# Kernel tuning notes

Measured on AMD Instinct MI355X. Metric: run time of the kernel, lower is better.

## Reference

```python
import math
import jax, jax.numpy as jnp
import numpy as np

QDEPTH = 8
WIDTH = 32
HEIGHT = 32
PIXELS = WIDTH * HEIGHT          # 1024
WIRES = int(math.ceil(math.log2(PIXELS)))  # 10, and PIXELS == 2**WIRES exactly
BATCH = 2048


def setup_inputs() -> dict:
    key = jax.random.key(0)
    k1, k2 = jax.random.split(key)
    x = jax.random.normal(k1, (BATCH, 1, WIDTH, HEIGHT), dtype=jnp.float32)
    # torch.randn(weight_shape) * 0.4
    weights = jax.random.normal(k2, (QDEPTH, WIRES, 3), dtype=jnp.float32) * 0.4
    return {"x": x, "weights": weights, "reps": 1}


def _apply_1q(s, U, wire):
    # s: (batch, 2, 2, ..., 2); apply 2x2 unitary U on qubit `wire` (axis wire+1)
    ax = wire + 1
    s = jnp.moveaxis(s, ax, -1)
    s = s @ U.T                      # new[..., i] = sum_j U[i, j] * old[..., j]
    return jnp.moveaxis(s, -1, ax)


def _apply_cnot(s, ctrl, tgt):
    # flip target bit on the control==1 half of the state
    c_ax = ctrl + 1
    t_ax = tgt + 1
    s0 = jnp.take(s, 0, axis=c_ax)
    s1 = jnp.take(s, 1, axis=c_ax)
    t = t_ax - 1 if t_ax > c_ax else t_ax
    s1 = jnp.flip(s1, axis=t)
    return jnp.stack([s0, s1], axis=c_ax)


def _rot_matrix(phi, theta, omega):
    # qml.Rot = RZ(phi) -> RY(theta) -> RZ(omega)
    c = jnp.cos(theta * 0.5)
    sn = jnp.sin(theta * 0.5)
    ep = jnp.exp(-0.5j * (phi + omega))   # e^{-i(phi+omega)/2}
    em = jnp.exp(-0.5j * (phi - omega))   # e^{-i(phi-omega)/2}
    return jnp.stack([
        jnp.stack([ep * c, -jnp.conj(em) * sn]),
        jnp.stack([em * sn, jnp.conj(ep) * c]),
    ]).astype(jnp.complex64)


def _circuit(psi, weights, reps):
    # psi: (batch, 2**WIRES) complex64 normalized state
    b = psi.shape[0]
    s = psi.reshape((b,) + (2,) * WIRES)
    w = jnp.tanh(weights)                 # qw_map.tanh
    # StronglyEntanglingLayers default ranges: r_l = l % (wires-1) + 1
    ranges = [(l % (WIRES - 1)) + 1 for l in range(QDEPTH)]
    for _ in range(reps):
        for l in range(QDEPTH):
            for q in range(WIRES):
                U = _rot_matrix(w[l, q, 0], w[l, q, 1], w[l, q, 2])
                s = _apply_1q(s, U, q)
            r = ranges[l]
            for q in range(WIRES):
                s = _apply_cnot(s, q, (q + r) % WIRES)
    return s.reshape(b, 2 ** WIRES)


def reference(x, weights, reps):
    b = x.shape[0]
    v = x.reshape(b, PIXELS)                       # b 1 w h -> b (w h)
    old_norm = jnp.linalg.norm(v, axis=-1, keepdims=True)
    psi = (v / old_norm).astype(jnp.complex64)     # real amplitudes, zero imag
    out = _circuit(psi, weights, reps)
    out = out * old_norm.astype(jnp.complex64)
    return out.reshape(b, 1, WIDTH, HEIGHT)
```

## Files before the change

kernel.cpp:

```cpp
#include <hip/hip_runtime.h>
#include <math.h>


#define WIRES   10
#define NSTATE  1024
#define QDEPTH  8
#define NBATCH  2048
#define NGATES  (QDEPTH * WIRES)

#define WS_WORDS 1280

__device__ __forceinline__ int perm_g(int j, int r) {
#pragma unroll
    for (int q = WIRES - 1; q >= 0; --q) {
        const int cb = 9 - q;
        const int tb = 9 - ((q + r) % WIRES);
        j ^= ((j >> cb) & 1) << tb;
    }
    return j;
}

__global__ __launch_bounds__(1024) void qprep(
    const float* __restrict__ weights, float* __restrict__ ws)
{
    const int tid = threadIdx.x;
    if (tid < NGATES) {
        const float phi   = tanhf(weights[tid * 3 + 0]);
        const float theta = tanhf(weights[tid * 3 + 1]);
        const float omega = tanhf(weights[tid * 3 + 2]);
        const float c  = cosf(theta * 0.5f);
        const float sn = sinf(theta * 0.5f);
        const float a  = 0.5f * (phi + omega);
        const float bb = 0.5f * (phi - omega);
        const float ca = cosf(a),  sa = sinf(a);
        const float cb = cosf(bb), sb = sinf(bb);
        ws[tid * 8 + 0] =  ca * c;  ws[tid * 8 + 1] = -sa * c;
        ws[tid * 8 + 2] = -cb * sn; ws[tid * 8 + 3] = -sb * sn;
        ws[tid * 8 + 4] =  cb * sn; ws[tid * 8 + 5] = -sb * sn;
        ws[tid * 8 + 6] =  ca * c;  ws[tid * 8 + 7] =  sa * c;
    }
    int* wsI = (int*)ws;
    if (tid >= 128 && tid < 256) {
        const int e = tid - 128, l = e >> 4, t = e & 15;
        const int j = perm_g(t, (l % (WIRES - 1)) + 1);
        wsI[640 + e] = ((j & 15) << 6) | (j >> 4);
    }
    if (tid >= 256 && tid < 768) {
        const int e = tid - 256, l = e >> 6, v = e & 63;
        const int j = perm_g(v << 4, (l % (WIRES - 1)) + 1);
        wsI[768 + e] = ((j & 15) << 6) | (j >> 4);
    }
}

template<int CTRL>
__device__ __forceinline__ float dppmov(float x) {
    return __int_as_float(__builtin_amdgcn_update_dpp(
        0, __float_as_int(x), CTRL, 0xF, 0xF, true));
}
#define FX1(v)  dppmov<0xB1>(v)
#define FX2(v)  dppmov<0x4E>(v)
#define FX4(v)  dppmov<0x1B>(dppmov<0x141>(v))
#define FX8(v)  dppmov<0x128>(v)
#define FX16(v) __shfl_xor((v), 16, 64)
#define FX32(v) __shfl_xor((v), 32, 64)

#define LANE_GATE(W, J, FETCH)                                                \
    {                                                                         \
        const float* __restrict__ u = gw + (W) * 8;                           \
        const bool hi = (lane >> (J)) & 1;                                    \
        const float c0r = hi ? u[6] : u[0], c0i = hi ? u[7] : u[1];           \
        const float c1r = hi ? u[4] : u[2], c1i = hi ? u[5] : u[3];           \
        _Pragma("unroll")                                                     \
        for (int t = 0; t < 16; ++t) {                                        \
            const float pr = FETCH(re[t]);                                    \
            const float pi = FETCH(im[t]);                                    \
            const float sr = re[t], si = im[t];                               \
            re[t] = c0r*sr - c0i*si + c1r*pr - c1i*pi;                        \
            im[t] = c0r*si + c0i*sr + c1r*pi + c1i*pr;                        \
        }                                                                     \
    }

__global__ __launch_bounds__(64) void qsim_wave(
    const float* __restrict__ x,
    const float* __restrict__ ws,
    float* __restrict__ out,
    const int interleaved)
{
    __shared__ float lre[NSTATE];
    __shared__ float lim[NSTATE];
    const int lane = threadIdx.x;
    const int b    = blockIdx.x;
    const int* __restrict__ wsI = (const int*)ws;

    float re[16], im[16];

    const float4* __restrict__ x4 =
        (const float4*)(x + ((size_t)b << 10) + (lane << 4));
#pragma unroll
    for (int k = 0; k < 4; ++k) {
        const float4 v = x4[k];
        re[4*k+0] = v.x; re[4*k+1] = v.y; re[4*k+2] = v.z; re[4*k+3] = v.w;
        im[4*k+0] = 0.f; im[4*k+1] = 0.f; im[4*k+2] = 0.f; im[4*k+3] = 0.f;
    }

    for (int l = 0; l < QDEPTH; ++l) {
        const float* __restrict__ gw = ws + l * 80;

#pragma unroll
        for (int bb = 0; bb < 4; ++bb) {
            const float* __restrict__ u = gw + (9 - bb) * 8;
            const float u00r = u[0], u00i = u[1], u01r = u[2], u01i = u[3];
            const float u10r = u[4], u10i = u[5], u11r = u[6], u11i = u[7];
#pragma unroll
            for (int t0 = 0; t0 < 16; ++t0) {
                if (t0 & (1 << bb)) continue;
                const int t1 = t0 | (1 << bb);
                const float a0r = re[t0], a0i = im[t0];
                const float a1r = re[t1], a1i = im[t1];
                re[t0] = u00r*a0r - u00i*a0i + u01r*a1r - u01i*a1i;
                im[t0] = u00r*a0i + u00i*a0r + u01r*a1i + u01i*a1r;
                re[t1] = u10r*a0r - u10i*a0i + u11r*a1r - u11i*a1i;
                im[t1] = u10r*a0i + u10i*a0r + u11r*a1i + u11i*a1r;
            }
        }

        LANE_GATE(5, 0, FX1)
        LANE_GATE(4, 1, FX2)
        LANE_GATE(3, 2, FX4)
        LANE_GATE(2, 3, FX8)
        LANE_GATE(1, 4, FX16)
        LANE_GATE(0, 5, FX32)

#pragma unroll
        for (int t = 0; t < 16; ++t) {
            lre[t * 64 + lane] = re[t];
            lim[t * 64 + lane] = im[t];
        }
        const int ga = wsI[768 + l * 64 + lane];
#pragma unroll
        for (int t = 0; t < 16; ++t) {
            const int a = ga ^ wsI[640 + l * 16 + t];
            re[t] = lre[a];
            im[t] = lim[a];
        }
    }

    if (interleaved) {
        float2* __restrict__ o2 = (float2*)out;
#pragma unroll
        for (int t = 0; t < 16; ++t)
            o2[((size_t)b << 10) + (lane << 4) + t] = make_float2(re[t], im[t]);
    } else {
        float4* __restrict__ o4 = (float4*)(out + ((size_t)b << 10) + (lane << 4));
#pragma unroll
        for (int k = 0; k < 4; ++k)
            o4[k] = make_float4(re[4*k+0], re[4*k+1], re[4*k+2], re[4*k+3]);
    }
}

__global__ __launch_bounds__(256) void qcircuit_kernel(
    const float* __restrict__ x, const float* __restrict__ weights,
    float* __restrict__ out, const int interleaved)
{
    __shared__ float s_re[NSTATE];
    __shared__ float s_im[NSTATE];
    __shared__ float s_g[NGATES][8];
    const int tid = threadIdx.x;
    const int b   = blockIdx.x;
    if (tid < NGATES) {
        const float phi   = tanhf(weights[tid * 3 + 0]);
        const float theta = tanhf(weights[tid * 3 + 1]);
        const float omega = tanhf(weights[tid * 3 + 2]);
        const float c  = cosf(theta * 0.5f);
        const float sn = sinf(theta * 0.5f);
        const float a  = 0.5f * (phi + omega);
        const float bb = 0.5f * (phi - omega);
        const float ca = cosf(a),  sa = sinf(a);
        const float cb = cosf(bb), sb = sinf(bb);
        s_g[tid][0] =  ca * c;  s_g[tid][1] = -sa * c;
        s_g[tid][2] = -cb * sn; s_g[tid][3] = -sb * sn;
        s_g[tid][4] =  cb * sn; s_g[tid][5] = -sb * sn;
        s_g[tid][6] =  ca * c;  s_g[tid][7] =  sa * c;
    }
#pragma unroll
    for (int k = 0; k < 4; ++k) {
        const int i = tid + 256 * k;
        s_re[i] = x[b * NSTATE + i];
        s_im[i] = 0.0f;
    }
    __syncthreads();
    for (int l = 0; l < QDEPTH; ++l) {
        for (int q = 0; q < WIRES; ++q) {
            const int gi = l * WIRES + q;
            const float u00r = s_g[gi][0], u00i = s_g[gi][1];
            const float u01r = s_g[gi][2], u01i = s_g[gi][3];
            const float u10r = s_g[gi][4], u10i = s_g[gi][5];
            const float u11r = s_g[gi][6], u11i = s_g[gi][7];
            const int sh = 9 - q;
            const int m  = 1 << sh;
#pragma unroll
            for (int k = 0; k < 2; ++k) {
                const int p  = tid + 256 * k;
                const int i0 = ((p >> sh) << (sh + 1)) | (p & (m - 1));
                const int i1 = i0 | m;
                const float a0r = s_re[i0], a0i = s_im[i0];
                const float a1r = s_re[i1], a1i = s_im[i1];
                s_re[i0] = u00r*a0r - u00i*a0i + u01r*a1r - u01i*a1i;
                s_im[i0] = u00r*a0i + u00i*a0r + u01r*a1i + u01i*a1r;
                s_re[i1] = u10r*a0r - u10i*a0i + u11r*a1r - u11i*a1i;
                s_im[i1] = u10r*a0i + u10i*a0r + u11r*a1i + u11i*a1r;
            }
            __syncthreads();
        }
        const int r = (l % (WIRES - 1)) + 1;
        float vr[4], vi[4];
#pragma unroll
        for (int k = 0; k < 4; ++k) {
            const int i = tid + 256 * k;
            const int j = perm_g(i, r);
            vr[k] = s_re[j]; vi[k] = s_im[j];
        }
        __syncthreads();
#pragma unroll
        for (int k = 0; k < 4; ++k) {
            const int i = tid + 256 * k;
            s_re[i] = vr[k]; s_im[i] = vi[k];
        }
        __syncthreads();
    }
    if (interleaved) {
#pragma unroll
        for (int k = 0; k < 4; ++k) {
            const int i  = tid + 256 * k;
            const int fi = 2 * (b * NSTATE + i);
            out[fi + 0] = s_re[i];
            out[fi + 1] = s_im[i];
        }
    } else {
#pragma unroll
        for (int k = 0; k < 4; ++k) {
            const int i = tid + 256 * k;
            out[b * NSTATE + i] = s_re[i];
        }
    }
}

extern "C" void kernel_launch(void* const* d_in, const int* in_sizes, int n_in,
                              void* d_out, int out_size, void* d_ws, size_t ws_size,
                              hipStream_t stream) {
    const float* x       = (const float*)d_in[0];
    const float* weights = (const float*)d_in[1];
    float* out = (float*)d_out;
    const int interleaved = (out_size >= 2 * NBATCH * NSTATE) ? 1 : 0;

    if (ws_size >= WS_WORDS * sizeof(float)) {
        float* ws = (float*)d_ws;
        qprep<<<1, 1024, 0, stream>>>(weights, ws);
        qsim_wave<<<NBATCH, 64, 0, stream>>>(x, ws, out, interleaved);
    } else {
        qcircuit_kernel<<<NBATCH, 256, 0, stream>>>(x, weights, out, interleaved);
    }
}
```

Baseline: 110.0 us.

## Split each batch state across two wavefronts with 8 amplitudes per lane

Each batch element's 1024-amplitude state is now split across two 64-lane wavefronts with 8 amplitudes per thread instead of 16. Gates on the low three qubits run in registers and the next six run as cross-lane DPP or shuffle swaps. The top qubit's gate is folded into the shared-memory CNOT permutation gather, which reads both partner amplitudes. The aim is to halve per-thread register pressure and raise parallelism per state, at the cost of block-wide syncthreads and extra LDS reads each layer. Output stores are also widened to float4 in the interleaved case.

After: 108.7 us. About the same (-1.2%).

```diff
diff --git a/kernel.cpp b/kernel.cpp
--- a/kernel.cpp
+++ b/kernel.cpp
@@ -8,7 +8,7 @@
 #define NBATCH  2048
 #define NGATES  (QDEPTH * WIRES)
 
-#define WS_WORDS 1280
+#define WS_WORDS 1728
 
 __device__ __forceinline__ int perm_g(int j, int r) {
 #pragma unroll
@@ -40,15 +40,14 @@
         ws[tid * 8 + 6] =  ca * c;  ws[tid * 8 + 7] =  sa * c;
     }
     int* wsI = (int*)ws;
-    if (tid >= 128 && tid < 256) {
-        const int e = tid - 128, l = e >> 4, t = e & 15;
-        const int j = perm_g(t, (l % (WIRES - 1)) + 1);
-        wsI[640 + e] = ((j & 15) << 6) | (j >> 4);
-    }
-    if (tid >= 256 && tid < 768) {
-        const int e = tid - 256, l = e >> 6, v = e & 63;
-        const int j = perm_g(v << 4, (l % (WIRES - 1)) + 1);
-        wsI[768 + e] = ((j & 15) << 6) | (j >> 4);
+    if (tid < 64) {
+        const int l = tid >> 3, t = tid & 7;
+        wsI[640 + tid] = perm_g(t, (l % (WIRES - 1)) + 1);
+    }
+    {
+        const int l = tid >> 7, e = tid & 127;
+        const int i0 = ((e >> 6) << 9) | ((e & 63) << 3);
+        wsI[704 + tid] = perm_g(i0, (l % (WIRES - 1)) + 1);
     }
 }
 
@@ -64,14 +63,32 @@
 #define FX16(v) __shfl_xor((v), 16, 64)
 #define FX32(v) __shfl_xor((v), 32, 64)
 
-#define LANE_GATE(W, J, FETCH)                                                \
+#define APPLY_LOCAL8(uptr, mask)                                              \
+    {                                                                         \
+        const float* __restrict__ u = (uptr);                                 \
+        const float u00r = u[0], u00i = u[1], u01r = u[2], u01i = u[3];       \
+        const float u10r = u[4], u10i = u[5], u11r = u[6], u11i = u[7];       \
+        _Pragma("unroll")                                                     \
+        for (int t0 = 0; t0 < 8; ++t0) {                                      \
+            if (t0 & (mask)) continue;                                        \
+            const int t1 = t0 | (mask);                                       \
+            const float a0r = re[t0], a0i = im[t0];                           \
+            const float a1r = re[t1], a1i = im[t1];                           \
+            re[t0] = u00r*a0r - u00i*a0i + u01r*a1r - u01i*a1i;               \
+            im[t0] = u00r*a0i + u00i*a0r + u01r*a1i + u01i*a1r;               \
+            re[t1] = u10r*a0r - u10i*a0i + u11r*a1r - u11i*a1i;               \
+            im[t1] = u10r*a0i + u10i*a0r + u11r*a1i + u11i*a1r;               \
+        }                                                                     \
+    }
+
+#define LANE_GATE8(W, J, FETCH)                                               \
     {                                                                         \
         const float* __restrict__ u = gw + (W) * 8;                           \
         const bool hi = (lane >> (J)) & 1;                                    \
         const float c0r = hi ? u[6] : u[0], c0i = hi ? u[7] : u[1];           \
         const float c1r = hi ? u[4] : u[2], c1i = hi ? u[5] : u[3];           \
         _Pragma("unroll")                                                     \
-        for (int t = 0; t < 16; ++t) {                                        \
+        for (int t = 0; t < 8; ++t) {                                         \
             const float pr = FETCH(re[t]);                                    \
             const float pi = FETCH(im[t]);                                    \
             const float sr = re[t], si = im[t];                               \
@@ -80,7 +97,7 @@
         }                                                                     \
     }
 
-__global__ __launch_bounds__(64) void qsim_wave(
+__global__ __launch_bounds__(128) void qsim2(
     const float* __restrict__ x,
     const float* __restrict__ ws,
     float* __restrict__ out,
@@ -88,73 +105,71 @@
 {
     __shared__ float lre[NSTATE];
     __shared__ float lim[NSTATE];
-    const int lane = threadIdx.x;
+    const int tid  = threadIdx.x;
+    const int lane = tid & 63;
     const int b    = blockIdx.x;
+    const int i0   = ((tid >> 6) << 9) | (lane << 3);
     const int* __restrict__ wsI = (const int*)ws;
 
-    float re[16], im[16];
+    float re[8], im[8];
 
     const float4* __restrict__ x4 =
-        (const float4*)(x + ((size_t)b << 10) + (lane << 4));
-#pragma unroll
-    for (int k = 0; k < 4; ++k) {
-        const float4 v = x4[k];
-        re[4*k+0] = v.x; re[4*k+1] = v.y; re[4*k+2] = v.z; re[4*k+3] = v.w;
-        im[4*k+0] = 0.f; im[4*k+1] = 0.f; im[4*k+2] = 0.f; im[4*k+3] = 0.f;
+        (const float4*)(x + ((size_t)b << 10) + i0);
+    {
+        const float4 v0 = x4[0], v1 = x4[1];
+        re[0]=v0.x; re[1]=v0.y; re[2]=v0.z; re[3]=v0.w;
+        re[4]=v1.x; re[5]=v1.y; re[6]=v1.z; re[7]=v1.w;
+#pragma unroll
+        for (int t = 0; t < 8; ++t) im[t] = 0.f;
     }
 
     for (int l = 0; l < QDEPTH; ++l) {
         const float* __restrict__ gw = ws + l * 80;
 
-#pragma unroll
-        for (int bb = 0; bb < 4; ++bb) {
-            const float* __restrict__ u = gw + (9 - bb) * 8;
-            const float u00r = u[0], u00i = u[1], u01r = u[2], u01i = u[3];
-            const float u10r = u[4], u10i = u[5], u11r = u[6], u11i = u[7];
-#pragma unroll
-            for (int t0 = 0; t0 < 16; ++t0) {
-                if (t0 & (1 << bb)) continue;
-                const int t1 = t0 | (1 << bb);
-                const float a0r = re[t0], a0i = im[t0];
-                const float a1r = re[t1], a1i = im[t1];
-                re[t0] = u00r*a0r - u00i*a0i + u01r*a1r - u01i*a1i;
-                im[t0] = u00r*a0i + u00i*a0r + u01r*a1i + u01i*a1r;
-                re[t1] = u10r*a0r - u10i*a0i + u11r*a1r - u11i*a1i;
-                im[t1] = u10r*a0i + u10i*a0r + u11r*a1i + u11i*a1r;
-            }
-        }
-
-        LANE_GATE(5, 0, FX1)
-        LANE_GATE(4, 1, FX2)
-        LANE_GATE(3, 2, FX4)
-        LANE_GATE(2, 3, FX8)
-        LANE_GATE(1, 4, FX16)
-        LANE_GATE(0, 5, FX32)
-
-#pragma unroll
-        for (int t = 0; t < 16; ++t) {
-            lre[t * 64 + lane] = re[t];
-            lim[t * 64 + lane] = im[t];
-        }
-        const int ga = wsI[768 + l * 64 + lane];
-#pragma unroll
-        for (int t = 0; t < 16; ++t) {
-            const int a = ga ^ wsI[640 + l * 16 + t];
-            re[t] = lre[a];
-            im[t] = lim[a];
-        }
+        APPLY_LOCAL8(gw + 9*8, 1)
+        APPLY_LOCAL8(gw + 8*8, 2)
+        APPLY_LOCAL8(gw + 7*8, 4)
+
+        LANE_GATE8(6, 0, FX1)
+        LANE_GATE8(5, 1, FX2)
+        LANE_GATE8(4, 2, FX4)
+        LANE_GATE8(3, 3, FX8)
+        LANE_GATE8(2, 4, FX16)
+        LANE_GATE8(1, 5, FX32)
+
+        *(float4*)&lre[i0]     = make_float4(re[0], re[1], re[2], re[3]);
+        *(float4*)&lre[i0 + 4] = make_float4(re[4], re[5], re[6], re[7]);
+        *(float4*)&lim[i0]     = make_float4(im[0], im[1], im[2], im[3]);
+        *(float4*)&lim[i0 + 4] = make_float4(im[4], im[5], im[6], im[7]);
+        __syncthreads();
+
+        const float* __restrict__ u0 = gw;
+        const int gl = wsI[704 + l * 128 + tid];
+#pragma unroll
+        for (int t = 0; t < 8; ++t) {
+            const int j  = gl ^ wsI[640 + l * 8 + t];
+            const int jp = j ^ 512;
+            const float sr = lre[j],  si = lim[j];
+            const float pr = lre[jp], pi = lim[jp];
+            const bool hib = (j >> 9) & 1;
+            const float c0r = hib ? u0[6] : u0[0], c0i = hib ? u0[7] : u0[1];
+            const float c1r = hib ? u0[4] : u0[2], c1i = hib ? u0[5] : u0[3];
+            re[t] = c0r*sr - c0i*si + c1r*pr - c1i*pi;
+            im[t] = c0r*si + c0i*sr + c1r*pi + c1i*pr;
+        }
+        __syncthreads();
     }
 
     if (interleaved) {
-        float2* __restrict__ o2 = (float2*)out;
-#pragma unroll
-        for (int t = 0; t < 16; ++t)
-            o2[((size_t)b << 10) + (lane << 4) + t] = make_float2(re[t], im[t]);
+        float4* __restrict__ o4 = (float4*)(out + 2 * (((size_t)b << 10) + i0));
+        o4[0] = make_float4(re[0], im[0], re[1], im[1]);
+        o4[1] = make_float4(re[2], im[2], re[3], im[3]);
+        o4[2] = make_float4(re[4], im[4], re[5], im[5]);
+        o4[3] = make_float4(re[6], im[6], re[7], im[7]);
     } else {
-        float4* __restrict__ o4 = (float4*)(out + ((size_t)b << 10) + (lane << 4));
-#pragma unroll
-        for (int k = 0; k < 4; ++k)
-            o4[k] = make_float4(re[4*k+0], re[4*k+1], re[4*k+2], re[4*k+3]);
+        float4* __restrict__ o4 = (float4*)(out + ((size_t)b << 10) + i0);
+        o4[0] = make_float4(re[0], re[1], re[2], re[3]);
+        o4[1] = make_float4(re[4], re[5], re[6], re[7]);
     }
 }
 
@@ -256,7 +271,7 @@
     if (ws_size >= WS_WORDS * sizeof(float)) {
         float* ws = (float*)d_ws;
         qprep<<<1, 1024, 0, stream>>>(weights, ws);
-        qsim_wave<<<NBATCH, 64, 0, stream>>>(x, ws, out, interleaved);
+        qsim2<<<NBATCH, 128, 0, stream>>>(x, ws, out, interleaved);
     } else {
         qcircuit_kernel<<<NBATCH, 256, 0, stream>>>(x, weights, out, interleaved);
     }
```
